# Kernel optimization log

Hardware: AMD Instinct MI355X
Metric: run time of the kernel (lower is better)

## Reference

```python
import jax, jax.numpy as jnp
import numpy as np
from jax import lax

HEADS = 8
DIM_HEAD = 64
DIM = HEADS * DIM_HEAD  # 512


def _dwconv(x_nchw, w):
    # depthwise 3x3, stride 1, pad 1 (SAME), groups = channels
    return lax.conv_general_dilated(
        x_nchw, w, window_strides=(1, 1), padding='SAME',
        feature_group_count=x_nchw.shape[1],
        dimension_numbers=('NCHW', 'OIHW', 'NCHW'))


def setup_inputs() -> dict:
    key = jax.random.key(0)
    ks = jax.random.split(key, 9)
    b, h, w, c = 4, 256, 256, DIM
    s = 1.0 / np.sqrt(c)
    return {
        'x_in':    jax.random.normal(ks[0], (b, h, w, c), jnp.float32),
        'Wq':      jax.random.normal(ks[1], (c, DIM), jnp.float32) * s,
        'Wk':      jax.random.normal(ks[2], (c, DIM), jnp.float32) * s,
        'Wv':      jax.random.normal(ks[3], (c, DIM), jnp.float32) * s,
        'rescale': jnp.ones((HEADS, 1, 1), jnp.float32),
        'proj_w':  jax.random.normal(ks[4], (DIM, c), jnp.float32) * s,
        'proj_b':  jnp.zeros((c,), jnp.float32),
        'conv1_w': jax.random.normal(ks[5], (c, 1, 3, 3), jnp.float32) * (1.0 / 3.0),
        'conv2_w': jax.random.normal(ks[6], (c, 1, 3, 3), jnp.float32) * (1.0 / 3.0),
    }


def reference(x_in, Wq, Wk, Wv, rescale, proj_w, proj_b, conv1_w, conv2_w):
    b, h, w, c = x_in.shape
    n = h * w
    x = x_in.reshape(b, n, c)
    q_inp = x @ Wq  # [b, n, heads*d]
    k_inp = x @ Wk
    v_inp = x @ Wv

    def heads_dn(t):  # [b, n, heads*d] -> [b, heads, d, n]
        return t.reshape(b, n, HEADS, DIM_HEAD).transpose(0, 2, 3, 1)

    q = heads_dn(q_inp)
    k = heads_dn(k_inp)
    v = heads_dn(v_inp)

    # L2-normalize along token axis (F.normalize, eps=1e-12)
    qn = q / jnp.maximum(jnp.linalg.norm(q, axis=-1, keepdims=True), 1e-12)
    kn = k / jnp.maximum(jnp.linalg.norm(k, axis=-1, keepdims=True), 1e-12)

    # channel attention: [b, heads, d, d]
    attn = jnp.einsum('bhdn,bhen->bhde', kn, qn) * rescale
    attn = jax.nn.softmax(attn, axis=-1)
    xo = jnp.einsum('bhde,bhen->bhdn', attn, v)  # [b, heads, d, n]

    xo = xo.transpose(0, 3, 1, 2).reshape(b, n, HEADS * DIM_HEAD)
    out_c = (xo @ proj_w + proj_b).reshape(b, h, w, c)

    # depthwise conv positional embedding on v_inp
    vp = v_inp.reshape(b, h, w, c).transpose(0, 3, 1, 2)  # NCHW
    vp = _dwconv(vp, conv1_w)
    vp = jax.nn.gelu(vp, approximate=False)
    vp = _dwconv(vp, conv2_w)
    out_p = vp.transpose(0, 2, 3, 1)

    return out_c + out_p
```

## Files before the change

### kernel.cpp

```cpp
#include <hip/hip_runtime.h>
#include <math.h>

typedef unsigned short u16;
typedef unsigned int   u32;
typedef __attribute__((ext_vector_type(4))) float f32x4;
typedef __attribute__((ext_vector_type(8))) short bf16x8;
typedef __attribute__((ext_vector_type(8))) u16   u16x8;

#define DEVI static __device__ __forceinline__

DEVI float bf2f(u16 a){ u32 u=((u32)a)<<16; float f; __builtin_memcpy(&f,&u,4); return f; }
DEVI u16 f2bf(float f){ u32 u; __builtin_memcpy(&u,&f,4); u=u+0x7fffu+((u>>16)&1u); return (u16)(u>>16); }

DEVI void gload16(const u16* src, u16* lds){
  __builtin_amdgcn_global_load_lds((const __attribute__((address_space(1))) u32*)src,
                                   (__attribute__((address_space(3))) u32*)lds, 16, 0, 0);
}

__global__ void k_wvt(const float* __restrict__ Wv, u16* __restrict__ WvT){
  int n = blockIdx.x;
  for (int k = threadIdx.x; k < 512; k += 256)
    WvT[(size_t)n*512 + k] = f2bf(Wv[(size_t)k*512 + n]);
}
__global__ void k_wrep(const float* __restrict__ w1, const float* __restrict__ w2, float* __restrict__ wt){
  int s = blockIdx.x/9, tap = blockIdx.x%9, c = threadIdx.x;
  const float* w = s ? w2 : w1;
  wt[(size_t)(s*9+tap)*512 + c] = w[(size_t)c*9 + tap];
}

__global__ __launch_bounds__(1024, 4) void k_gemm_v(const float* __restrict__ x, const u16* __restrict__ WvT,
                                                    u16* __restrict__ v, u16* __restrict__ xbT){
  __shared__ __align__(16) u16 Al[128*64];
  __shared__ __align__(16) u16 Bl[512*64];
  const int tid = threadIdx.x;
  const int l = tid & 63, w = tid >> 6;
  const int wr = w >> 3, wc = w & 7;
  const long r0 = (long)blockIdx.x * 128;
  f32x4 acc[4][4] = {};
  for (int k0 = 0; k0 < 512; k0 += 64){
    {
      int row = tid >> 3, c = tid & 7;
      const float* xp = x + (r0 + row)*512 + k0 + c*8;
      f32x4 va = *(const f32x4*)xp, vb = *(const f32x4*)(xp+4);
      u16x8 o;
      o[0]=f2bf(va.x); o[1]=f2bf(va.y); o[2]=f2bf(va.z); o[3]=f2bf(va.w);
      o[4]=f2bf(vb.x); o[5]=f2bf(vb.y); o[6]=f2bf(vb.z); o[7]=f2bf(vb.w);
      *(u16x8*)&Al[row*64 + ((c ^ (row&7))*8)] = o;
    }
    #pragma unroll
    for (int i = 0; i < 4; ++i){
      int blkrow = w*32 + i*8;
      int r = blkrow + (l>>3);
      const u16* src = WvT + (size_t)r*512 + k0 + (((l&7) ^ ((l>>3)&7))*8);
      gload16(src, &Bl[blkrow*64]);
    }
    __syncthreads();
    #pragma unroll
    for (int ks = 0; ks < 2; ++ks){
      bf16x8 af[4], bfr[4];
      #pragma unroll
      for (int mf = 0; mf < 4; ++mf){
        int row = wr*64 + mf*16 + (l&15);
        af[mf] = *(const bf16x8*)&Al[row*64 + (((ks*4 + (l>>4)) ^ (row&7))*8)];
      }
      #pragma unroll
      for (int nf = 0; nf < 4; ++nf){
        int row = wc*64 + nf*16 + (l&15);
        bfr[nf] = *(const bf16x8*)&Bl[row*64 + (((ks*4 + (l>>4)) ^ (row&7))*8)];
      }
      #pragma unroll
      for (int mf = 0; mf < 4; ++mf)
        #pragma unroll
        for (int nf = 0; nf < 4; ++nf)
          acc[mf][nf] = __builtin_amdgcn_mfma_f32_16x16x32_bf16(af[mf], bfr[nf], acc[mf][nf], 0,0,0);
    }
    {
      int chloc = tid & 63, tg = tid >> 6;
      u16x8 o;
      #pragma unroll
      for (int j = 0; j < 8; ++j){
        int tok = tg*8 + j;
        o[j] = Al[tok*64 + (((chloc>>3) ^ (tok&7))*8) + (chloc&7)];
      }
      *(u16x8*)(xbT + (size_t)(k0 + chloc)*262144 + r0 + tg*8) = o;
    }
    __syncthreads();
  }
  #pragma unroll
  for (int mf = 0; mf < 4; ++mf)
    #pragma unroll
    for (int nf = 0; nf < 4; ++nf){
      int col = wc*64 + nf*16 + (l&15);
      #pragma unroll
      for (int j = 0; j < 4; ++j){
        long row = r0 + wr*64 + mf*16 + (l>>4)*4 + j;
        v[(size_t)row*512 + col] = f2bf(acc[mf][nf][j]);
      }
    }
}

__global__ __launch_bounds__(1024, 4) void k_syrk(const u16* __restrict__ xbT, float* __restrict__ P){
  __shared__ __align__(16) u16 AL[256*64];
  __shared__ __align__(16) u16 BL[256*64];
  const int bid = blockIdx.x;
  const int cs = bid & 63, combo = (bid>>6)%3, b = bid/192;
  const int hA = (combo==2) ? 1 : 0;
  const int tid = threadIdx.x;
  const int l = tid & 63, w = tid>>6, wi = w>>2, wj = w&3;
  const long tokb0 = (long)b*65536 + (long)cs*1024;
  const u16* Bread = (combo==1) ? BL : AL;
  f32x4 acc[4][4] = {};
  for (int st = 0; st < 16; ++st){
    const long tokb = tokb0 + st*64;
    #pragma unroll
    for (int i = 0; i < 2; ++i){
      int blkrow = w*16 + i*8;
      int r = blkrow + (l>>3);
      const u16* src = xbT + (size_t)(hA*256 + r)*262144 + tokb + (((l&7) ^ ((l>>3)&7))*8);
      gload16(src, &AL[blkrow*64]);
    }
    if (combo == 1){
      #pragma unroll
      for (int i = 0; i < 2; ++i){
        int blkrow = w*16 + i*8;
        int r = blkrow + (l>>3);
        const u16* src = xbT + (size_t)(256 + r)*262144 + tokb + (((l&7) ^ ((l>>3)&7))*8);
        gload16(src, &BL[blkrow*64]);
      }
    }
    __syncthreads();
    #pragma unroll
    for (int ks = 0; ks < 2; ++ks){
      bf16x8 af[4], bfr[4];
      #pragma unroll
      for (int mf = 0; mf < 4; ++mf){
        int row = wi*64 + mf*16 + (l&15);
        af[mf] = *(const bf16x8*)&AL[row*64 + (((ks*4 + (l>>4)) ^ (row&7))*8)];
      }
      #pragma unroll
      for (int nf = 0; nf < 4; ++nf){
        int row = wj*64 + nf*16 + (l&15);
        bfr[nf] = *(const bf16x8*)&Bread[row*64 + (((ks*4 + (l>>4)) ^ (row&7))*8)];
      }
      #pragma unroll
      for (int mf = 0; mf < 4; ++mf)
        #pragma unroll
        for (int nf = 0; nf < 4; ++nf)
          acc[mf][nf] = __builtin_amdgcn_mfma_f32_16x16x32_bf16(af[mf], bfr[nf], acc[mf][nf], 0,0,0);
    }
    __syncthreads();
  }
  float* Pb = P + (size_t)bid*65536;
  #pragma unroll
  for (int mf = 0; mf < 4; ++mf)
    #pragma unroll
    for (int nf = 0; nf < 4; ++nf)
      #pragma unroll
      for (int j = 0; j < 4; ++j){
        int il = wi*64 + mf*16 + (l>>4)*4 + j;
        int jl = wj*64 + nf*16 + (l&15);
        Pb[il*256 + jl] = acc[mf][nf][j];
      }
}

__global__ void k_sred(const float* __restrict__ P, float* __restrict__ S){
  int bid = blockIdx.x;
  int il = bid & 255, combo = (bid>>8)%3, b = bid/768;
  int hi = (combo==2)?1:0, hj = (combo==0)?0:1;
  int jl = threadIdx.x;
  float s = 0.f;
  for (int cs = 0; cs < 64; ++cs)
    s += P[((size_t)(b*192 + combo*64 + cs))*65536 + il*256 + jl];
  int I = hi*256 + il, J = hj*256 + jl;
  S[((size_t)b*512 + I)*512 + J] = s;
  if (combo == 1) S[((size_t)b*512 + J)*512 + I] = s;
}

__global__ __launch_bounds__(256) void k_a1(const float* __restrict__ S, const float* __restrict__ Wq,
                                            const float* __restrict__ Wk, float* __restrict__ T, float* __restrict__ U){
  int bid = blockIdx.x;
  int b = bid>>6, rem = bid&63, which = rem>>5, rbase = (rem&31)*16;
  const float* W = which ? Wk : Wq;
  float* O = which ? U : T;
  int tid = threadIdx.x;
  int rg = tid>>6, c0 = (tid&63)*8;
  const float* Sr = S + (size_t)b*262144 + (size_t)(rbase + rg*4)*512;
  float acc[4][8] = {};
  for (int k = 0; k < 512; ++k){
    float s0 = Sr[k], s1 = Sr[512+k], s2 = Sr[1024+k], s3 = Sr[1536+k];
    f32x4 wa = *(const f32x4*)(W + (size_t)k*512 + c0);
    f32x4 wb = *(const f32x4*)(W + (size_t)k*512 + c0 + 4);
    #pragma unroll
    for (int j = 0; j < 4; ++j){
      acc[0][j]   += s0*wa[j]; acc[1][j]   += s1*wa[j]; acc[2][j]   += s2*wa[j]; acc[3][j]   += s3*wa[j];
      acc[0][4+j] += s0*wb[j]; acc[1][4+j] += s1*wb[j]; acc[2][4+j] += s2*wb[j]; acc[3][4+j] += s3*wb[j];
    }
  }
  float* Ob = O + (size_t)b*262144;
  #pragma unroll
  for (int i = 0; i < 4; ++i){
    f32x4 o0, o1;
    o0.x=acc[i][0]; o0.y=acc[i][1]; o0.z=acc[i][2]; o0.w=acc[i][3];
    o1.x=acc[i][4]; o1.y=acc[i][5]; o1.z=acc[i][6]; o1.w=acc[i][7];
    *(f32x4*)(Ob + (size_t)(rbase+rg*4+i)*512 + c0)     = o0;
    *(f32x4*)(Ob + (size_t)(rbase+rg*4+i)*512 + c0 + 4) = o1;
  }
}

__global__ void k_a2(const float* __restrict__ Wq, const float* __restrict__ Wk,
                     const float* __restrict__ T, const float* __restrict__ U,
                     float* __restrict__ G, float* __restrict__ q2, float* __restrict__ k2){
  int b = blockIdx.x>>3, h = blockIdx.x&7;
  int tid = threadIdx.x;
  int d0 = (tid>>4)*4, e0 = (tid&15)*4;
  const float* Tb = T + (size_t)b*262144;
  float acc[4][4] = {};
  for (int i = 0; i < 512; ++i){
    f32x4 wk = *(const f32x4*)(Wk + (size_t)i*512 + h*64 + d0);
    f32x4 tv = *(const f32x4*)(Tb + (size_t)i*512 + h*64 + e0);
    #pragma unroll
    for (int di = 0; di < 4; ++di)
      #pragma unroll
      for (int ej = 0; ej < 4; ++ej) acc[di][ej] += wk[di]*tv[ej];
  }
  float* Gb = G + ((size_t)(b*8+h))*4096;
  #pragma unroll
  for (int di = 0; di < 4; ++di)
    #pragma unroll
    for (int ej = 0; ej < 4; ++ej) Gb[(d0+di)*64 + e0+ej] = acc[di][ej];
  if (tid < 64){
    int e = tid; float a = 0.f;
    for (int j = 0; j < 512; ++j) a += Wq[(size_t)j*512 + h*64 + e] * Tb[(size_t)j*512 + h*64 + e];
    q2[b*512 + h*64 + e] = a;
  } else if (tid < 128){
    int d = tid - 64; float a = 0.f;
    const float* Ub = U + (size_t)b*262144;
    for (int j = 0; j < 512; ++j) a += Wk[(size_t)j*512 + h*64 + d] * Ub[(size_t)j*512 + h*64 + d];
    k2[b*512 + h*64 + d] = a;
  }
}

__global__ void k_a3(const float* __restrict__ G, const float* __restrict__ resc,
                     const float* __restrict__ q2, const float* __restrict__ k2, float* __restrict__ Aa){
  int b = blockIdx.x>>3, h = blockIdx.x&7;
  int d = threadIdx.x;
  const float* g = G + ((size_t)(b*8+h))*4096 + d*64;
  float kn = fmaxf(sqrtf(k2[b*512 + h*64 + d]), 1e-12f);
  float sc = resc[h] / kn;
  float m = -3.4e38f;
  for (int e = 0; e < 64; ++e){
    float qn = fmaxf(sqrtf(q2[b*512 + h*64 + e]), 1e-12f);
    m = fmaxf(m, g[e]*sc/qn);
  }
  float ssum = 0.f;
  for (int e = 0; e < 64; ++e){
    float qn = fmaxf(sqrtf(q2[b*512 + h*64 + e]), 1e-12f);
    ssum += expf(g[e]*sc/qn - m);
  }
  float inv = 1.0f/ssum;
  float* ao = Aa + ((size_t)(b*8+h))*4096 + d*64;
  for (int e = 0; e < 64; ++e){
    float qn = fmaxf(sqrtf(q2[b*512 + h*64 + e]), 1e-12f);
    ao[e] = expf(g[e]*sc/qn - m)*inv;
  }
}

__global__ void k_a4(const float* __restrict__ Aa, const float* __restrict__ pw, u16* __restrict__ MT){
  int bid = blockIdx.x;
  int jt = bid&3, h = (bid>>2)&7, b = bid>>5;
  int tid = threadIdx.x;
  int j = jt*128 + (tid&127), eh = tid>>7;
  const float* Ab = Aa + ((size_t)(b*8+h))*4096;
  float acc[32] = {};
  for (int d = 0; d < 64; ++d){
    float p = pw[(size_t)(h*64+d)*512 + j];
    const float* ar = Ab + d*64 + eh*32;
    #pragma unroll
    for (int q = 0; q < 8; ++q){
      f32x4 pa = *(const f32x4*)(ar + q*4);
      acc[q*4+0] += pa.x*p; acc[q*4+1] += pa.y*p; acc[q*4+2] += pa.z*p; acc[q*4+3] += pa.w*p;
    }
  }
  u16* mo = MT + (size_t)b*262144 + (size_t)j*512 + h*64 + eh*32;
  #pragma unroll
  for (int q = 0; q < 16; ++q){
    u32 pk = (u32)f2bf(acc[2*q]) | ((u32)f2bf(acc[2*q+1])<<16);
    *(u32*)&mo[2*q] = pk;
  }
}

__global__ __launch_bounds__(256) void k_conv_fused(const u16* __restrict__ v, const float* __restrict__ wt,
                                                    u16* __restrict__ cbuf){
  __shared__ u16 vt[400*32];
  __shared__ u16 t1[324*32];
  const int bid = blockIdx.x;
  const int g = bid & 15, tx = (bid>>4)&15, ty = (bid>>8)&15, b = bid>>12;
  const int c0 = g*32, oy0 = ty*16, ox0 = tx*16;
  const int tid = threadIdx.x;
  const int ch8 = tid & 3;

  for (int k = 0; k < 7; ++k){
    int q = tid + k*256; if (q >= 1600) break;
    int pos = q >> 2, c8 = q & 3;
    int ly = pos / 20, lx = pos - ly*20;
    int gy = oy0 - 2 + ly, gx = ox0 - 2 + lx;
    u16x8 val = {};
    if (gy >= 0 && gy < 256 && gx >= 0 && gx < 256)
      val = *(const u16x8*)(v + ((size_t)(b*65536 + gy*256 + gx))*512 + c0 + c8*8);
    *(u16x8*)&vt[pos*32 + c8*8] = val;
  }

  f32x4 wa[9], wb[9];
  #pragma unroll
  for (int tap = 0; tap < 9; ++tap){
    const float* wp = wt + (size_t)tap*512 + c0 + ch8*8;
    wa[tap] = *(const f32x4*)wp; wb[tap] = *(const f32x4*)(wp+4);
  }
  __syncthreads();

  for (int k = 0; k < 6; ++k){
    int q = tid + k*256; if (q >= 1296) break;
    int pos = q >> 2;
    int y1 = pos / 18, x1 = pos - y1*18;
    int gy1 = oy0 - 1 + y1, gx1 = ox0 - 1 + x1;
    bool inimg = (gy1 >= 0 && gy1 < 256 && gx1 >= 0 && gx1 < 256);
    float acc[8] = {};
    #pragma unroll
    for (int tap = 0; tap < 9; ++tap){
      int dy = tap/3, dx = tap - dy*3;
      u16x8 vv = *(const u16x8*)&vt[((y1+dy)*20 + x1+dx)*32 + ch8*8];
      #pragma unroll
      for (int j = 0; j < 8; ++j) acc[j] += bf2f(vv[j]) * (j<4 ? wa[tap][j] : wb[tap][j-4]);
    }
    u16x8 o;
    #pragma unroll
    for (int j = 0; j < 8; ++j){
      float a = acc[j];
      o[j] = inimg ? f2bf(0.5f*a*(1.0f + erff(a*0.70710678118654752f))) : (u16)0;
    }
    *(u16x8*)&t1[pos*32 + ch8*8] = o;
  }

  #pragma unroll
  for (int tap = 0; tap < 9; ++tap){
    const float* wp = wt + (size_t)(9+tap)*512 + c0 + ch8*8;
    wa[tap] = *(const f32x4*)wp; wb[tap] = *(const f32x4*)(wp+4);
  }
  __syncthreads();

  #pragma unroll
  for (int k = 0; k < 4; ++k){
    int q = tid + k*256;
    int pos = q >> 2;
    int y2 = pos >> 4, x2 = pos & 15;
    float acc[8] = {};
    #pragma unroll
    for (int tap = 0; tap < 9; ++tap){
      int dy = tap/3, dx = tap - dy*3;
      u16x8 tt = *(const u16x8*)&t1[((y2+dy)*18 + (x2+dx))*32 + ch8*8];
      #pragma unroll
      for (int j = 0; j < 8; ++j) acc[j] += bf2f(tt[j]) * (j<4 ? wa[tap][j] : wb[tap][j-4]);
    }
    u16x8 o;
    #pragma unroll
    for (int j = 0; j < 8; ++j) o[j] = f2bf(acc[j]);
    size_t tok = (size_t)b*65536 + (size_t)(oy0+y2)*256 + (ox0+x2);
    *(u16x8*)(cbuf + tok*512 + c0 + ch8*8) = o;
  }
}

__global__ __launch_bounds__(512) void k_gemm_out(const u16* __restrict__ v, const u16* __restrict__ MT,
                                                  const float* __restrict__ proj_b, const u16* __restrict__ cbuf,
                                                  float* __restrict__ out){
  __shared__ __align__(16) u16 Al[128*64];
  __shared__ __align__(16) u16 Bl[256*64];
  const int tid = threadIdx.x;
  const int l = tid & 63, w = tid >> 6;
  const int wr = w >> 2, wc = w & 3;
  const int bid = blockIdx.x;
  const int wg = (bid & 7)*512 + (bid >> 3);
  const long r0 = (long)(wg >> 1) * 128;
  const int  c0b = (wg & 1) * 256;
  const int  b = (int)(r0 >> 16);
  const u16* Mb = MT + (size_t)b*262144;
  f32x4 acc[4][4] = {};
  for (int k0 = 0; k0 < 512; k0 += 64){
    #pragma unroll
    for (int i = 0; i < 2; ++i){
      int blkrow = w*16 + i*8;
      int r = blkrow + (l>>3);
      const u16* src = v + (size_t)(r0 + r)*512 + k0 + (((l&7) ^ (r&7))*8);
      gload16(src, &Al[blkrow*64]);
    }
    #pragma unroll
    for (int i = 0; i < 4; ++i){
      int blkrow = w*32 + i*8;
      int r = blkrow + (l>>3);
      const u16* src = Mb + (size_t)(c0b + r)*512 + k0 + (((l&7) ^ (r&7))*8);
      gload16(src, &Bl[blkrow*64]);
    }
    __syncthreads();
    #pragma unroll
    for (int ks = 0; ks < 2; ++ks){
      bf16x8 af[4], bfr[4];
      #pragma unroll
      for (int mf = 0; mf < 4; ++mf){
        int row = wr*64 + mf*16 + (l&15);
        af[mf] = *(const bf16x8*)&Al[row*64 + (((ks*4 + (l>>4)) ^ (row&7))*8)];
      }
      #pragma unroll
      for (int nf = 0; nf < 4; ++nf){
        int row = wc*64 + nf*16 + (l&15);
        bfr[nf] = *(const bf16x8*)&Bl[row*64 + (((ks*4 + (l>>4)) ^ (row&7))*8)];
      }
      #pragma unroll
      for (int mf = 0; mf < 4; ++mf)
        #pragma unroll
        for (int nf = 0; nf < 4; ++nf)
          acc[mf][nf] = __builtin_amdgcn_mfma_f32_16x16x32_bf16(af[mf], bfr[nf], acc[mf][nf], 0,0,0);
    }
    __syncthreads();
  }
  #pragma unroll
  for (int mf = 0; mf < 4; ++mf)
    #pragma unroll
    for (int nf = 0; nf < 4; ++nf){
      int col = c0b + wc*64 + nf*16 + (l&15);
      float pb = proj_b[col];
      #pragma unroll
      for (int j = 0; j < 4; ++j){
        long row = r0 + wr*64 + mf*16 + (l>>4)*4 + j;
        out[(size_t)row*512 + col] = acc[mf][nf][j] + pb + bf2f(cbuf[(size_t)row*512 + col]);
      }
    }
}

extern "C" void kernel_launch(void* const* d_in, const int* in_sizes, int n_in,
                              void* d_out, int out_size, void* d_ws, size_t ws_size,
                              hipStream_t stream){
  const float* x   = (const float*)d_in[0];
  const float* Wq  = (const float*)d_in[1];
  const float* Wk  = (const float*)d_in[2];
  const float* Wv  = (const float*)d_in[3];
  const float* rsc = (const float*)d_in[4];
  const float* pw  = (const float*)d_in[5];
  const float* pb  = (const float*)d_in[6];
  const float* w1  = (const float*)d_in[7];
  const float* w2  = (const float*)d_in[8];
  float* out = (float*)d_out;
  char* ws = (char*)d_ws;

  const size_t MB256 = 268435456;
  u16*   v    = (u16*)ws;
  u16*   xbT  = (u16*)(ws + MB256);
  u16*   cbuf = xbT;
  char*  sm0  = ws + 2*MB256;
  float* P    = (float*)d_out;

  float* S   = (float*)(sm0);
  float* Tm  = (float*)(sm0 + 4194304);
  float* Um  = (float*)(sm0 + 8388608);
  float* G   = (float*)(sm0 + 12582912);
  float* Aa  = (float*)(sm0 + 13107200);
  float* q2  = (float*)(sm0 + 13631488);
  float* k2  = (float*)(sm0 + 13639680);
  u16*   MT  = (u16*)  (sm0 + 13647872);
  u16*   WvT = (u16*)  (sm0 + 15745024);
  float* wt  = (float*)(sm0 + 16269312);

  k_wvt <<<512, 256, 0, stream>>>(Wv, WvT);
  k_wrep<<<18, 512, 0, stream>>>(w1, w2, wt);
  k_gemm_v<<<2048, 1024, 0, stream>>>(x, WvT, v, xbT);
  k_syrk<<<768, 1024, 0, stream>>>(xbT, P);
  k_sred<<<3072, 256, 0, stream>>>(P, S);
  k_a1<<<256, 256, 0, stream>>>(S, Wq, Wk, Tm, Um);
  k_a2<<<32, 256, 0, stream>>>(Wq, Wk, Tm, Um, G, q2, k2);
  k_a3<<<32, 64, 0, stream>>>(G, rsc, q2, k2, Aa);
  k_a4<<<128, 256, 0, stream>>>(Aa, pw, MT);
  k_conv_fused<<<16384, 256, 0, stream>>>(v, wt, cbuf);
  k_gemm_out<<<4096, 512, 0, stream>>>(v, MT, pb, cbuf, out);
}
```

Before: 1.590 ms.

## Double-buffer output GEMM, use fp32 LDS tiles and tanh-GELU in conv

The output GEMM now double-buffers its A and B LDS tiles, so the global-to-LDS loads for the next K step are issued while MFMAs run on the current one. The fused depthwise conv is split into 16-channel groups, doubling the grid, and keeps its LDS tiles in fp32 so bf16 conversions leave the inner loops. It also swaps the exact erf GELU for the tanh approximation built on __expf. That approximation changes numerics against the exact-GELU reference, and the double buffering doubles LDS use per block, which can lower occupancy.

```diff
diff --git a/kernel.cpp b/kernel.cpp
--- a/kernel.cpp
+++ b/kernel.cpp
@@ -6,6 +6,7 @@
 typedef __attribute__((ext_vector_type(4))) float f32x4;
 typedef __attribute__((ext_vector_type(8))) short bf16x8;
 typedef __attribute__((ext_vector_type(8))) u16   u16x8;
+typedef __attribute__((ext_vector_type(4))) u16   u16x4;
 
 #define DEVI static __device__ __forceinline__
 
@@ -291,31 +292,31 @@
 
 __global__ __launch_bounds__(256) void k_conv_fused(const u16* __restrict__ v, const float* __restrict__ wt,
                                                     u16* __restrict__ cbuf){
-  __shared__ u16 vt[400*32];
-  __shared__ u16 t1[324*32];
+  __shared__ float vtf[400*16];
+  __shared__ float t1f[324*16];
   const int bid = blockIdx.x;
-  const int g = bid & 15, tx = (bid>>4)&15, ty = (bid>>8)&15, b = bid>>12;
-  const int c0 = g*32, oy0 = ty*16, ox0 = tx*16;
+  const int g = bid & 31, tx = (bid>>5)&15, ty = (bid>>9)&15, b = bid>>13;
+  const int c0 = g*16, oy0 = ty*16, ox0 = tx*16;
   const int tid = threadIdx.x;
-  const int ch8 = tid & 3;
+  const int quad = tid & 3;
 
   for (int k = 0; k < 7; ++k){
     int q = tid + k*256; if (q >= 1600) break;
-    int pos = q >> 2, c8 = q & 3;
+    int pos = q >> 2;
     int ly = pos / 20, lx = pos - ly*20;
     int gy = oy0 - 2 + ly, gx = ox0 - 2 + lx;
-    u16x8 val = {};
-    if (gy >= 0 && gy < 256 && gx >= 0 && gx < 256)
-      val = *(const u16x8*)(v + ((size_t)(b*65536 + gy*256 + gx))*512 + c0 + c8*8);
-    *(u16x8*)&vt[pos*32 + c8*8] = val;
-  }
-
-  f32x4 wa[9], wb[9];
-  #pragma unroll
-  for (int tap = 0; tap < 9; ++tap){
-    const float* wp = wt + (size_t)tap*512 + c0 + ch8*8;
-    wa[tap] = *(const f32x4*)wp; wb[tap] = *(const f32x4*)(wp+4);
-  }
+    f32x4 val = {};
+    if (gy >= 0 && gy < 256 && gx >= 0 && gx < 256){
+      u16x4 raw = *(const u16x4*)(v + ((size_t)(b*65536 + gy*256 + gx))*512 + c0 + quad*4);
+      val.x = bf2f(raw[0]); val.y = bf2f(raw[1]); val.z = bf2f(raw[2]); val.w = bf2f(raw[3]);
+    }
+    *(f32x4*)&vtf[pos*16 + quad*4] = val;
+  }
+
+  f32x4 wq[9];
+  #pragma unroll
+  for (int tap = 0; tap < 9; ++tap)
+    wq[tap] = *(const f32x4*)(wt + (size_t)tap*512 + c0 + quad*4);
   __syncthreads();
 
   for (int k = 0; k < 6; ++k){
@@ -324,28 +325,28 @@
     int y1 = pos / 18, x1 = pos - y1*18;
     int gy1 = oy0 - 1 + y1, gx1 = ox0 - 1 + x1;
     bool inimg = (gy1 >= 0 && gy1 < 256 && gx1 >= 0 && gx1 < 256);
-    float acc[8] = {};
+    const float* base = &vtf[(y1*20 + x1)*16 + quad*4];
+    float acc[4] = {};
     #pragma unroll
     for (int tap = 0; tap < 9; ++tap){
       int dy = tap/3, dx = tap - dy*3;
-      u16x8 vv = *(const u16x8*)&vt[((y1+dy)*20 + x1+dx)*32 + ch8*8];
-      #pragma unroll
-      for (int j = 0; j < 8; ++j) acc[j] += bf2f(vv[j]) * (j<4 ? wa[tap][j] : wb[tap][j-4]);
-    }
-    u16x8 o;
-    #pragma unroll
-    for (int j = 0; j < 8; ++j){
+      f32x4 vv = *(const f32x4*)(base + (dy*20 + dx)*16);
+      #pragma unroll
+      for (int j = 0; j < 4; ++j) acc[j] += vv[j]*wq[tap][j];
+    }
+    f32x4 o;
+    #pragma unroll
+    for (int j = 0; j < 4; ++j){
       float a = acc[j];
-      o[j] = inimg ? f2bf(0.5f*a*(1.0f + erff(a*0.70710678118654752f))) : (u16)0;
-    }
-    *(u16x8*)&t1[pos*32 + ch8*8] = o;
-  }
-
-  #pragma unroll
-  for (int tap = 0; tap < 9; ++tap){
-    const float* wp = wt + (size_t)(9+tap)*512 + c0 + ch8*8;
-    wa[tap] = *(const f32x4*)wp; wb[tap] = *(const f32x4*)(wp+4);
-  }
+      float gl = a / (1.0f + __expf(-1.5957691216f*a*(1.0f + 0.044715f*a*a)));
+      o[j] = inimg ? gl : 0.0f;
+    }
+    *(f32x4*)&t1f[pos*16 + quad*4] = o;
+  }
+
+  #pragma unroll
+  for (int tap = 0; tap < 9; ++tap)
+    wq[tap] = *(const f32x4*)(wt + (size_t)(9+tap)*512 + c0 + quad*4);
   __syncthreads();
 
   #pragma unroll
@@ -353,27 +354,28 @@
     int q = tid + k*256;
     int pos = q >> 2;
     int y2 = pos >> 4, x2 = pos & 15;
-    float acc[8] = {};
+    const float* base = &t1f[(y2*18 + x2)*16 + quad*4];
+    float acc[4] = {};
     #pragma unroll
     for (int tap = 0; tap < 9; ++tap){
       int dy = tap/3, dx = tap - dy*3;
-      u16x8 tt = *(const u16x8*)&t1[((y2+dy)*18 + (x2+dx))*32 + ch8*8];
-      #pragma unroll
-      for (int j = 0; j < 8; ++j) acc[j] += bf2f(tt[j]) * (j<4 ? wa[tap][j] : wb[tap][j-4]);
-    }
-    u16x8 o;
-    #pragma unroll
-    for (int j = 0; j < 8; ++j) o[j] = f2bf(acc[j]);
+      f32x4 tt = *(const f32x4*)(base + (dy*18 + dx)*16);
+      #pragma unroll
+      for (int j = 0; j < 4; ++j) acc[j] += tt[j]*wq[tap][j];
+    }
+    u16x4 o;
+    #pragma unroll
+    for (int j = 0; j < 4; ++j) o[j] = f2bf(acc[j]);
     size_t tok = (size_t)b*65536 + (size_t)(oy0+y2)*256 + (ox0+x2);
-    *(u16x8*)(cbuf + tok*512 + c0 + ch8*8) = o;
+    *(u16x4*)(cbuf + tok*512 + c0 + quad*4) = o;
   }
 }
 
 __global__ __launch_bounds__(512) void k_gemm_out(const u16* __restrict__ v, const u16* __restrict__ MT,
                                                   const float* __restrict__ proj_b, const u16* __restrict__ cbuf,
                                                   float* __restrict__ out){
-  __shared__ __align__(16) u16 Al[128*64];
-  __shared__ __align__(16) u16 Bl[256*64];
+  __shared__ __align__(16) u16 Al[2][128*64];
+  __shared__ __align__(16) u16 Bl[2][256*64];
   const int tid = threadIdx.x;
   const int l = tid & 63, w = tid >> 6;
   const int wr = w >> 2, wc = w & 3;
@@ -384,34 +386,41 @@
   const int  b = (int)(r0 >> 16);
   const u16* Mb = MT + (size_t)b*262144;
   f32x4 acc[4][4] = {};
-  for (int k0 = 0; k0 < 512; k0 += 64){
+
+  auto STAGE = [&](int buf, int k0){
     #pragma unroll
     for (int i = 0; i < 2; ++i){
       int blkrow = w*16 + i*8;
       int r = blkrow + (l>>3);
       const u16* src = v + (size_t)(r0 + r)*512 + k0 + (((l&7) ^ (r&7))*8);
-      gload16(src, &Al[blkrow*64]);
+      gload16(src, &Al[buf][blkrow*64]);
     }
     #pragma unroll
     for (int i = 0; i < 4; ++i){
       int blkrow = w*32 + i*8;
       int r = blkrow + (l>>3);
       const u16* src = Mb + (size_t)(c0b + r)*512 + k0 + (((l&7) ^ (r&7))*8);
-      gload16(src, &Bl[blkrow*64]);
-    }
-    __syncthreads();
+      gload16(src, &Bl[buf][blkrow*64]);
+    }
+  };
+
+  STAGE(0, 0);
+  __syncthreads();
+  for (int t = 0; t < 8; ++t){
+    const int cur = t & 1;
+    if (t < 7) STAGE(cur^1, (t+1)*64);
     #pragma unroll
     for (int ks = 0; ks < 2; ++ks){
       bf16x8 af[4], bfr[4];
       #pragma unroll
       for (int mf = 0; mf < 4; ++mf){
         int row = wr*64 + mf*16 + (l&15);
-        af[mf] = *(const bf16x8*)&Al[row*64 + (((ks*4 + (l>>4)) ^ (row&7))*8)];
+        af[mf] = *(const bf16x8*)&Al[cur][row*64 + (((ks*4 + (l>>4)) ^ (row&7))*8)];
       }
       #pragma unroll
       for (int nf = 0; nf < 4; ++nf){
         int row = wc*64 + nf*16 + (l&15);
-        bfr[nf] = *(const bf16x8*)&Bl[row*64 + (((ks*4 + (l>>4)) ^ (row&7))*8)];
+        bfr[nf] = *(const bf16x8*)&Bl[cur][row*64 + (((ks*4 + (l>>4)) ^ (row&7))*8)];
       }
       #pragma unroll
       for (int mf = 0; mf < 4; ++mf)
@@ -477,6 +486,6 @@
   k_a2<<<32, 256, 0, stream>>>(Wq, Wk, Tm, Um, G, q2, k2);
   k_a3<<<32, 64, 0, stream>>>(G, rsc, q2, k2, Aa);
   k_a4<<<128, 256, 0, stream>>>(Aa, pw, MT);
-  k_conv_fused<<<16384, 256, 0, stream>>>(v, wt, cbuf);
+  k_conv_fused<<<32768, 256, 0, stream>>>(v, wt, cbuf);
   k_gemm_out<<<4096, 512, 0, stream>>>(v, MT, pb, cbuf, out);
 }
```

After: 1.627 ms. 2.3% more time.
